# Kernel tuning notes

Measured on AMD Instinct MI355X. Metric: run time of the kernel, lower is better.

Reference implementation:

```python
import jax, jax.numpy as jnp
import numpy as np

CUTOFF_RATIO = 4
FS = 8000.0
ZEROS = 8
HALF = int(ZEROS * CUTOFF_RATIO / 2)          # 16
FILTER_SIZE = 2 * HALF + 1                     # 33


def _sinc(x):
    # sin(x)/x with safe gradient at 0 (input NOT multiplied by pi)
    xs = jnp.where(x == 0, 1.0, x)
    return jnp.where(x == 0, 1.0, jnp.sin(xs) / xs)


def _filters(n, alpha, beta):
    # per-timestep cutoff: (pi/r + alpha*sin(beta*t/fs)) / (2*pi)   -> (n,)
    t = jnp.arange(n, dtype=jnp.float32)
    cutoff = (jnp.pi / CUTOFF_RATIO + alpha * jnp.sin(beta * t / FS)) / (2.0 * jnp.pi)
    # hann window, periodic=False, length FILTER_SIZE
    k = jnp.arange(FILTER_SIZE, dtype=jnp.float32)
    window = 0.5 - 0.5 * jnp.cos(2.0 * jnp.pi * k / (FILTER_SIZE - 1))
    time = jnp.arange(-HALF, HALF + 1, dtype=jnp.float32)
    f = 2.0 * cutoff[:, None] * window[None, :] * _sinc(2.0 * jnp.pi * cutoff[:, None] * time[None, :])
    f = f / f.sum(axis=-1, keepdims=True)      # (n, FILTER_SIZE)
    return f[:, ::-1]                           # flipped, as in compute_conv_mat


def setup_inputs() -> dict:
    key = jax.random.key(0)
    k1, k2, k3 = jax.random.split(key, 3)
    x = jax.random.normal(k1, (64, 32768), dtype=jnp.float32)
    alpha = jax.random.uniform(k2, (), dtype=jnp.float32) * 0.5   # keep cutoff_t > 0
    beta = jax.random.uniform(k3, (), dtype=jnp.float32) * 4.0
    return {"input": x, "alpha": alpha, "beta": beta}


def reference(input, alpha, beta):
    # Time-varying FIR: identical math to building the (n, n) banded conv_mat
    # (rows t cover original cols t..t+filter_size-1, then sliced to cols
    # half_size..n+half_size-1) followed by matmul -- without the n^2 matrix.
    n = input.shape[-1]
    filt = _filters(n, alpha, beta)                              # (n, K)
    xpad = jnp.pad(input, ((0, 0), (HALF, HALF)))                # (B, n+2*HALF)
    idx = jnp.arange(n)[:, None] + jnp.arange(FILTER_SIZE)[None, :]  # (n, K)
    windows = xpad[:, idx]                                       # (B, n, K)
    return jnp.einsum('tk,btk->bt', filt, windows)
```

## Files before the change

### kernel.cpp

```cpp
#include <hip/hip_runtime.h>
#include <math.h>


constexpr int   HALF  = 16;
constexpr int   BLOCK = 256;
constexpr int   VEC   = 4;
constexpr int   ROWS  = 2;
constexpr float PI_F  = 3.14159265358979323846f;
constexpr double PI_D = 3.14159265358979323846;

constexpr float W_TAB[16] = {
    0.0f,
    (float)((0.5 + 0.5 *  0.98078528040323044) / (PI_D *  1.0)),
    (float)((0.5 + 0.5 *  0.92387953251128674) / (PI_D *  2.0)),
    (float)((0.5 + 0.5 *  0.83146961230254524) / (PI_D *  3.0)),
    (float)((0.5 + 0.5 *  0.70710678118654752) / (PI_D *  4.0)),
    (float)((0.5 + 0.5 *  0.55557023301960222) / (PI_D *  5.0)),
    (float)((0.5 + 0.5 *  0.38268343236508977) / (PI_D *  6.0)),
    (float)((0.5 + 0.5 *  0.19509032201612827) / (PI_D *  7.0)),
    (float)((0.5 + 0.5 *  0.0                ) / (PI_D *  8.0)),
    (float)((0.5 + 0.5 * -0.19509032201612827) / (PI_D *  9.0)),
    (float)((0.5 + 0.5 * -0.38268343236508977) / (PI_D * 10.0)),
    (float)((0.5 + 0.5 * -0.55557023301960222) / (PI_D * 11.0)),
    (float)((0.5 + 0.5 * -0.70710678118654752) / (PI_D * 12.0)),
    (float)((0.5 + 0.5 * -0.83146961230254524) / (PI_D * 13.0)),
    (float)((0.5 + 0.5 * -0.92387953251128674) / (PI_D * 14.0)),
    (float)((0.5 + 0.5 * -0.98078528040323044) / (PI_D * 15.0)),
};

template <bool CHECK>
__device__ __forceinline__ void lpf_body(const float* __restrict__ x,
                                         float* __restrict__ out,
                                         float alpha, float beta,
                                         int n, int t0, int row0)
{
    float C[VEC][16];
    #pragma unroll
    for (int o = 0; o < VEC; ++o) {
        const float tf    = (float)(t0 + o);
        const float theta = 0.25f * PI_F + alpha * sinf(beta * tf * (1.0f / 8000.0f));
        float s1, c1;
        sincosf(theta, &s1, &c1);

        float f[16];
        f[0] = theta * (float)(1.0 / PI_D);
        f[1] = s1 * W_TAB[1];
        const float two_c = 2.0f * c1;
        float skm1 = s1, skm2 = 0.0f;
        #pragma unroll
        for (int k = 2; k < 16; ++k) {
            const float sk = fmaf(two_c, skm1, -skm2);
            f[k] = sk * W_TAB[k];
            skm2 = skm1; skm1 = sk;
        }
        float sum = f[0];
        #pragma unroll
        for (int k = 1; k < 16; ++k) sum += 2.0f * f[k];
        const float inv = 1.0f / sum;
        #pragma unroll
        for (int k = 0; k < 16; ++k) C[o][k] = f[k] * inv;
    }

    #pragma unroll
    for (int r = 0; r < ROWS; ++r) {
        const float* __restrict__ base = x + (size_t)(row0 + r) * (size_t)n;
        float w[36];
        if (CHECK) {
            #pragma unroll
            for (int i = 0; i < 36; ++i) {
                const int idx = t0 - 16 + i;
                w[i] = (idx >= 0 && idx < n) ? base[idx] : 0.0f;
            }
        } else {
            const float4* __restrict__ p = (const float4*)(base + t0 - 16);
            #pragma unroll
            for (int q = 0; q < 9; ++q) {
                const float4 v = p[q];
                w[4*q+0] = v.x; w[4*q+1] = v.y; w[4*q+2] = v.z; w[4*q+3] = v.w;
            }
        }

        float4 res;
        float* rp = &res.x;
        #pragma unroll
        for (int o = 0; o < VEC; ++o) {
            const int ci = o + 16;
            float acc = C[o][0] * w[ci];
            #pragma unroll
            for (int k = 1; k < 16; ++k)
                acc = fmaf(C[o][k], w[ci - k] + w[ci + k], acc);
            rp[o] = acc;
        }
        *(float4*)(out + (size_t)(row0 + r) * (size_t)n + t0) = res;
    }
}

__global__ __launch_bounds__(BLOCK)
void LowPassFilter_53661321396356_kernel(const float* __restrict__ x,
                                         const float* __restrict__ alpha_p,
                                         const float* __restrict__ beta_p,
                                         float* __restrict__ out,
                                         int n)
{
    const int t0 = (blockIdx.x * BLOCK + threadIdx.x) * VEC;
    if (t0 >= n) return;
    const int row0   = blockIdx.y * ROWS;
    const float alpha = alpha_p[0];
    const float beta  = beta_p[0];

    if (blockIdx.x == 0 || blockIdx.x == gridDim.x - 1) {
        lpf_body<true >(x, out, alpha, beta, n, t0, row0);
    } else {
        lpf_body<false>(x, out, alpha, beta, n, t0, row0);
    }
}

extern "C" void kernel_launch(void* const* d_in, const int* in_sizes, int n_in,
                              void* d_out, int out_size, void* d_ws, size_t ws_size,
                              hipStream_t stream) {
    const float* x       = (const float*)d_in[0];
    const float* alpha_p = (const float*)d_in[1];
    const float* beta_p  = (const float*)d_in[2];
    float*       out     = (float*)d_out;

    const int B = 64;
    const int n = in_sizes[0] / B;

    dim3 grid((n + BLOCK * VEC - 1) / (BLOCK * VEC), B / ROWS);
    dim3 block(BLOCK);
    LowPassFilter_53661321396356_kernel<<<grid, block, 0, stream>>>(
        x, alpha_p, beta_p, out, n);
}
```

Baseline: 24.29 us.

## Precompute per-timestep filter coefficients in a separate kernel via workspace

Splits the work into two kernels. The first computes the 16 symmetric coefficients per timestep once and writes them to the workspace in k-major layout. The second, the FIR kernel, loads them as float4, so the trig and normalisation are no longer repeated for each of the 32 row-pair blocks. It also switches to fast __sinf/__cosf intrinsics, which costs some accuracy, and it adds a second launch plus about 2 MB of extra coefficient traffic.

```diff
diff --git a/kernel.cpp b/kernel.cpp
--- a/kernel.cpp
+++ b/kernel.cpp
@@ -2,7 +2,6 @@
 #include <math.h>
 
 
-constexpr int   HALF  = 16;
 constexpr int   BLOCK = 256;
 constexpr int   VEC   = 4;
 constexpr int   ROWS  = 2;
@@ -28,38 +27,50 @@
     (float)((0.5 + 0.5 * -0.98078528040323044) / (PI_D * 15.0)),
 };
 
+__global__ __launch_bounds__(BLOCK)
+void lpf_coef_kernel(const float* __restrict__ alpha_p,
+                     const float* __restrict__ beta_p,
+                     float* __restrict__ cw, int n)
+{
+    const int t = blockIdx.x * BLOCK + threadIdx.x;
+    if (t >= n) return;
+    const float alpha = alpha_p[0];
+    const float beta  = beta_p[0];
+
+    const float theta = 0.25f * PI_F + alpha * __sinf(beta * (float)t * (1.0f / 8000.0f));
+    const float s1 = __sinf(theta);
+    const float c1 = __cosf(theta);
+
+    float f[16];
+    f[0] = theta * (float)(1.0 / PI_D);
+    f[1] = s1 * W_TAB[1];
+    const float two_c = 2.0f * c1;
+    float skm1 = s1, skm2 = 0.0f;
+    #pragma unroll
+    for (int k = 2; k < 16; ++k) {
+        const float sk = fmaf(two_c, skm1, -skm2);
+        f[k] = sk * W_TAB[k];
+        skm2 = skm1; skm1 = sk;
+    }
+    float sum = f[0];
+    #pragma unroll
+    for (int k = 1; k < 16; ++k) sum += 2.0f * f[k];
+    const float inv = 1.0f / sum;
+    #pragma unroll
+    for (int k = 0; k < 16; ++k)
+        cw[(size_t)k * (size_t)n + t] = f[k] * inv;
+}
+
 template <bool CHECK>
-__device__ __forceinline__ void lpf_body(const float* __restrict__ x,
+__device__ __forceinline__ void fir_body(const float* __restrict__ x,
+                                         const float* __restrict__ cw,
                                          float* __restrict__ out,
-                                         float alpha, float beta,
                                          int n, int t0, int row0)
 {
-    float C[VEC][16];
+    float4 ck[16];
     #pragma unroll
-    for (int o = 0; o < VEC; ++o) {
-        const float tf    = (float)(t0 + o);
-        const float theta = 0.25f * PI_F + alpha * sinf(beta * tf * (1.0f / 8000.0f));
-        float s1, c1;
-        sincosf(theta, &s1, &c1);
-
-        float f[16];
-        f[0] = theta * (float)(1.0 / PI_D);
-        f[1] = s1 * W_TAB[1];
-        const float two_c = 2.0f * c1;
-        float skm1 = s1, skm2 = 0.0f;
-        #pragma unroll
-        for (int k = 2; k < 16; ++k) {
-            const float sk = fmaf(two_c, skm1, -skm2);
-            f[k] = sk * W_TAB[k];
-            skm2 = skm1; skm1 = sk;
-        }
-        float sum = f[0];
-        #pragma unroll
-        for (int k = 1; k < 16; ++k) sum += 2.0f * f[k];
-        const float inv = 1.0f / sum;
-        #pragma unroll
-        for (int k = 0; k < 16; ++k) C[o][k] = f[k] * inv;
-    }
+    for (int k = 0; k < 16; ++k)
+        ck[k] = *(const float4*)(cw + (size_t)k * (size_t)n + t0);
 
     #pragma unroll
     for (int r = 0; r < ROWS; ++r) {
@@ -82,13 +93,14 @@
 
         float4 res;
         float* rp = &res.x;
+        const float* cp = &ck[0].x;
         #pragma unroll
         for (int o = 0; o < VEC; ++o) {
             const int ci = o + 16;
-            float acc = C[o][0] * w[ci];
+            float acc = cp[o] * w[ci];
             #pragma unroll
             for (int k = 1; k < 16; ++k)
-                acc = fmaf(C[o][k], w[ci - k] + w[ci + k], acc);
+                acc = fmaf(cp[k*4 + o], w[ci - k] + w[ci + k], acc);
             rp[o] = acc;
         }
         *(float4*)(out + (size_t)(row0 + r) * (size_t)n + t0) = res;
@@ -96,22 +108,18 @@
 }
 
 __global__ __launch_bounds__(BLOCK)
-void LowPassFilter_53661321396356_kernel(const float* __restrict__ x,
-                                         const float* __restrict__ alpha_p,
-                                         const float* __restrict__ beta_p,
-                                         float* __restrict__ out,
-                                         int n)
+void lpf_fir_kernel(const float* __restrict__ x,
+                    const float* __restrict__ cw,
+                    float* __restrict__ out, int n)
 {
     const int t0 = (blockIdx.x * BLOCK + threadIdx.x) * VEC;
     if (t0 >= n) return;
-    const int row0   = blockIdx.y * ROWS;
-    const float alpha = alpha_p[0];
-    const float beta  = beta_p[0];
+    const int row0 = blockIdx.y * ROWS;
 
     if (blockIdx.x == 0 || blockIdx.x == gridDim.x - 1) {
-        lpf_body<true >(x, out, alpha, beta, n, t0, row0);
+        fir_body<true >(x, cw, out, n, t0, row0);
     } else {
-        lpf_body<false>(x, out, alpha, beta, n, t0, row0);
+        fir_body<false>(x, cw, out, n, t0, row0);
     }
 }
 
@@ -122,12 +130,14 @@
     const float* alpha_p = (const float*)d_in[1];
     const float* beta_p  = (const float*)d_in[2];
     float*       out     = (float*)d_out;
+    float*       cw      = (float*)d_ws;
 
     const int B = 64;
     const int n = in_sizes[0] / B;
 
-    dim3 grid((n + BLOCK * VEC - 1) / (BLOCK * VEC), B / ROWS);
-    dim3 block(BLOCK);
-    LowPassFilter_53661321396356_kernel<<<grid, block, 0, stream>>>(
-        x, alpha_p, beta_p, out, n);
+    dim3 cgrid((n + BLOCK - 1) / BLOCK);
+    lpf_coef_kernel<<<cgrid, dim3(BLOCK), 0, stream>>>(alpha_p, beta_p, cw, n);
+
+    dim3 fgrid((n + BLOCK * VEC - 1) / (BLOCK * VEC), B / ROWS);
+    lpf_fir_kernel<<<fgrid, dim3(BLOCK), 0, stream>>>(x, cw, out, n);
 }
```

After: 29.44 us. +21.2%, slower.
